# Kernel tuning notes

Measured on AMD Instinct MI355X. Metric: run time of the kernel, lower is better.

## Reference

```python
import jax, jax.numpy as jnp
import numpy as np

NUM_VIEWS = 11

def setup_inputs() -> dict:
    key = jax.random.key(0)
    ks = jax.random.split(key, 6)
    BF, T, D_IN, D_OUT, R = 128, 196, 1024, 1024, 4
    B = 16
    x = jax.random.normal(ks[0], (BF, T, D_IN), dtype=jnp.float32)
    view_idx = jax.random.randint(ks[1], (B,), 0, NUM_VIEWS)
    W = jax.random.normal(ks[2], (D_OUT, D_IN), dtype=jnp.float32) * (1.0 / np.sqrt(D_IN))
    b = jax.random.normal(ks[3], (D_OUT,), dtype=jnp.float32) * 0.01
    lora_A = jax.random.normal(ks[4], (NUM_VIEWS, D_IN, R), dtype=jnp.float32) * (1.0 / np.sqrt(D_IN))
    lora_B = jax.random.normal(ks[5], (NUM_VIEWS, R, D_OUT), dtype=jnp.float32) * 0.02
    return {"x": x, "view_idx": view_idx, "W": W, "b": b, "lora_A": lora_A, "lora_B": lora_B}

def reference(x, view_idx, W, b, lora_A, lora_B):
    # base linear: [BF, T, D_in] @ [D_in, D_out]
    out = jnp.einsum('bti,oi->bto', x, W) + b
    BF = x.shape[0]
    B = view_idx.shape[0]
    if BF != B:  # static shapes -> Python branch is jit-safe
        curr = jnp.repeat(view_idx, BF // B)  # expand per-frame view index
    else:
        curr = view_idx
    curr = jnp.clip(curr, 0, NUM_VIEWS - 1)
    A = lora_A[curr]          # [BF, D_in, R] gathered per sample
    Bm = lora_B[curr]         # [BF, R, D_out]
    h = jnp.einsum('bti,bir->btr', x, A)      # low-rank projection
    lora = jnp.einsum('btr,bro->bto', h, Bm)  # back to D_out
    return out + lora
```

## Files before the change

kernel.cpp:

```cpp
#include <hip/hip_runtime.h>
#include <hip/hip_bf16.h>
#include <stdint.h>

#define M_TOT 25088
#define N_TOT 1024
#define K_TOT 1024
#define NVIEW 11
#define ROWS_PER_VIEW 1568

#define BM 128
#define BN 128

typedef unsigned short u16;
typedef __bf16 bf16x8 __attribute__((ext_vector_type(8)));
typedef float f32x4 __attribute__((ext_vector_type(4)));
typedef unsigned short u16x4 __attribute__((ext_vector_type(4)));

#define AS1 __attribute__((address_space(1)))
#define AS3 __attribute__((address_space(3)))

#define XB_ELEMS ((size_t)M_TOT * K_TOT)
#define WB_ELEMS ((size_t)N_TOT * K_TOT)
#define WB_OFF_B (XB_ELEMS * 2)
#define H_OFF_B  (WB_OFF_B + WB_ELEMS * 2)
#define WS_NEEDED (H_OFF_B + (size_t)M_TOT * 4 * 4)

__device__ __forceinline__ u16 f2bf(float f) {
    union { float f; unsigned int i; } c; c.f = f;
    unsigned int i = c.i;
    return (u16)((i + 0x7FFFu + ((i >> 16) & 1u)) >> 16);
}

__global__ __launch_bounds__(256) void prep_kernel(
    const float* __restrict__ x, const float* __restrict__ W,
    const int* __restrict__ view_idx, const float* __restrict__ lora_A,
    u16* __restrict__ xb, u16* __restrict__ wb, float* __restrict__ h) {
    const int wave = threadIdx.x >> 6;
    const int lane = threadIdx.x & 63;
    const int blk  = blockIdx.x;

    if (blk >= M_TOT / 4) {
        const int row = (blk - M_TOT / 4) * 4 + wave;
        const float* src = W + (size_t)row * K_TOT;
        u16* dst = wb + (size_t)row * K_TOT;
#pragma unroll
        for (int it = 0; it < 4; ++it) {
            const int k = it * 256 + lane * 4;
            float4 v = *(const float4*)(src + k);
            u16x4 o = { f2bf(v.x), f2bf(v.y), f2bf(v.z), f2bf(v.w) };
            *(u16x4*)(dst + k) = o;
        }
        return;
    }

    const int row = blk * 4 + wave;
    int v = view_idx[row / ROWS_PER_VIEW];
    v = v < 0 ? 0 : (v > NVIEW - 1 ? NVIEW - 1 : v);
    const float* A  = lora_A + (size_t)v * (K_TOT * 4);
    const float* xr = x + (size_t)row * K_TOT;
    u16* dst = xb + (size_t)row * K_TOT;

    float a0 = 0.f, a1 = 0.f, a2 = 0.f, a3 = 0.f;
#pragma unroll
    for (int it = 0; it < 4; ++it) {
        const int k = it * 256 + lane * 4;
        float4 xv = *(const float4*)(xr + k);
        u16x4 o = { f2bf(xv.x), f2bf(xv.y), f2bf(xv.z), f2bf(xv.w) };
        *(u16x4*)(dst + k) = o;
        float4 av0 = *(const float4*)(A + (size_t)(k + 0) * 4);
        float4 av1 = *(const float4*)(A + (size_t)(k + 1) * 4);
        float4 av2 = *(const float4*)(A + (size_t)(k + 2) * 4);
        float4 av3 = *(const float4*)(A + (size_t)(k + 3) * 4);
        a0 += xv.x * av0.x + xv.y * av1.x + xv.z * av2.x + xv.w * av3.x;
        a1 += xv.x * av0.y + xv.y * av1.y + xv.z * av2.y + xv.w * av3.y;
        a2 += xv.x * av0.z + xv.y * av1.z + xv.z * av2.z + xv.w * av3.z;
        a3 += xv.x * av0.w + xv.y * av1.w + xv.z * av2.w + xv.w * av3.w;
    }
#pragma unroll
    for (int off = 32; off > 0; off >>= 1) {
        a0 += __shfl_xor(a0, off, 64);
        a1 += __shfl_xor(a1, off, 64);
        a2 += __shfl_xor(a2, off, 64);
        a3 += __shfl_xor(a3, off, 64);
    }
    if (lane == 0)
        *(float4*)(h + (size_t)row * 4) = make_float4(a0, a1, a2, a3);
}

__global__ __launch_bounds__(256) void h_only_kernel(
    const float* __restrict__ x, const int* __restrict__ view_idx,
    const float* __restrict__ lora_A, float* __restrict__ h) {
    const int row  = blockIdx.x * 4 + (threadIdx.x >> 6);
    const int lane = threadIdx.x & 63;
    int v = view_idx[row / ROWS_PER_VIEW];
    v = v < 0 ? 0 : (v > NVIEW - 1 ? NVIEW - 1 : v);
    const float* A  = lora_A + (size_t)v * (K_TOT * 4);
    const float* xr = x + (size_t)row * K_TOT;
    float a0 = 0.f, a1 = 0.f, a2 = 0.f, a3 = 0.f;
#pragma unroll
    for (int it = 0; it < 4; ++it) {
        const int k = it * 256 + lane * 4;
        float4 xv = *(const float4*)(xr + k);
        float4 av0 = *(const float4*)(A + (size_t)(k + 0) * 4);
        float4 av1 = *(const float4*)(A + (size_t)(k + 1) * 4);
        float4 av2 = *(const float4*)(A + (size_t)(k + 2) * 4);
        float4 av3 = *(const float4*)(A + (size_t)(k + 3) * 4);
        a0 += xv.x * av0.x + xv.y * av1.x + xv.z * av2.x + xv.w * av3.x;
        a1 += xv.x * av0.y + xv.y * av1.y + xv.z * av2.y + xv.w * av3.y;
        a2 += xv.x * av0.z + xv.y * av1.z + xv.z * av2.z + xv.w * av3.z;
        a3 += xv.x * av0.w + xv.y * av1.w + xv.z * av2.w + xv.w * av3.w;
    }
#pragma unroll
    for (int off = 32; off > 0; off >>= 1) {
        a0 += __shfl_xor(a0, off, 64);
        a1 += __shfl_xor(a1, off, 64);
        a2 += __shfl_xor(a2, off, 64);
        a3 += __shfl_xor(a3, off, 64);
    }
    if (lane == 0)
        *(float4*)(h + (size_t)row * 4) = make_float4(a0, a1, a2, a3);
}

__device__ __forceinline__ void stage32(const u16* __restrict__ gA,
                                        const u16* __restrict__ gB,
                                        u16* lA, u16* lB, int kofs, int tid) {
#pragma unroll
    for (int i = 0; i < 2; ++i) {
        const int e  = i * 2048 + tid * 8;
        const int r  = e >> 5;
        const int cc = tid & 3;
        const int c  = ((cc ^ ((r >> 1) & 3)) << 3);
        __builtin_amdgcn_global_load_lds(
            (const AS1 void*)(gA + (size_t)r * K_TOT + kofs + c),
            (AS3 void*)(lA + e), 16, 0, 0);
        __builtin_amdgcn_global_load_lds(
            (const AS1 void*)(gB + (size_t)r * K_TOT + kofs + c),
            (AS3 void*)(lB + e), 16, 0, 0);
    }
}

__global__ __launch_bounds__(256, 3) void gemm_bf16_kernel(
    const u16* __restrict__ xb, const u16* __restrict__ wb,
    const float* __restrict__ bias, const int* __restrict__ view_idx,
    const float* __restrict__ lora_B, const float* __restrict__ h,
    float* __restrict__ out) {
    __shared__ u16 As[2][BM * 32];
    __shared__ u16 Bs[2][BN * 32];

    const int tid = threadIdx.x;
    const int id = blockIdx.x;
    int bx, by;
    if (id < 1536) { const int c = id >> 6, w = id & 63; by = c * 8 + (w & 7); bx = w >> 3; }
    else           { const int r = id - 1536; by = 192 + (r & 3); bx = r >> 2; }

    const int lane = tid & 63;
    const int wave = tid >> 6;
    const int wm   = (wave >> 1) * 64;
    const int wn   = (wave & 1) * 64;
    const int l16  = lane & 15;
    const int quad = lane >> 4;
    const int sw2  = (l16 >> 1) & 3;
    const int csw  = ((quad ^ sw2) << 3);

    const u16* gA = xb + (size_t)(by * BM) * K_TOT;
    const u16* gB = wb + (size_t)(bx * BN) * K_TOT;

    f32x4 acc[4][4] = {};

    stage32(gA, gB, &As[0][0], &Bs[0][0], 0, tid);
    __syncthreads();

    #pragma unroll 2
    for (int kt = 0; kt < K_TOT / 32; ++kt) {
        const int buf  = kt & 1;
        const int nbuf = buf ^ 1;

        if (kt + 1 < K_TOT / 32)
            stage32(gA, gB, &As[nbuf][0], &Bs[nbuf][0], (kt + 1) * 32, tid);

        bf16x8 a_frag[4], b_frag[4];
#pragma unroll
        for (int mi = 0; mi < 4; ++mi)
            a_frag[mi] = *(const bf16x8*)(const void*)(
                &As[buf][0] + (wm + mi * 16 + l16) * 32 + csw);
#pragma unroll
        for (int ni = 0; ni < 4; ++ni)
            b_frag[ni] = *(const bf16x8*)(const void*)(
                &Bs[buf][0] + (wn + ni * 16 + l16) * 32 + csw);
#pragma unroll
        for (int mi = 0; mi < 4; ++mi)
#pragma unroll
            for (int ni = 0; ni < 4; ++ni)
                acc[mi][ni] = __builtin_amdgcn_mfma_f32_16x16x32_bf16(
                    a_frag[mi], b_frag[ni], acc[mi][ni], 0, 0, 0);

        __syncthreads();
    }

    const int rowBase = by * BM + wm;
    const int colBase = bx * BN + wn;
    float biasv[4];
#pragma unroll
    for (int ni = 0; ni < 4; ++ni) biasv[ni] = bias[colBase + ni * 16 + l16];

    const int ve0 = (by * BM) / ROWS_PER_VIEW;
    const int ve1 = (by * BM + BM - 1) / ROWS_PER_VIEW;
    if (ve0 == ve1) {
        int v = view_idx[ve0];
        v = v < 0 ? 0 : (v > NVIEW - 1 ? NVIEW - 1 : v);
        const float* Bv = lora_B + (size_t)v * (4 * N_TOT);
        float Bvv[4][4];
#pragma unroll
        for (int r = 0; r < 4; ++r)
#pragma unroll
            for (int ni = 0; ni < 4; ++ni)
                Bvv[r][ni] = Bv[r * N_TOT + colBase + ni * 16 + l16];
#pragma unroll
        for (int mi = 0; mi < 4; ++mi) {
#pragma unroll
            for (int reg = 0; reg < 4; ++reg) {
                const int grow = rowBase + mi * 16 + quad * 4 + reg;
                const float4 hv = *(const float4*)(h + (size_t)grow * 4);
                float* orow = out + (size_t)grow * N_TOT;
#pragma unroll
                for (int ni = 0; ni < 4; ++ni) {
                    float lora = hv.x * Bvv[0][ni] + hv.y * Bvv[1][ni]
                               + hv.z * Bvv[2][ni] + hv.w * Bvv[3][ni];
                    orow[colBase + ni * 16 + l16] = acc[mi][ni][reg] + biasv[ni] + lora;
                }
            }
        }
    } else {
#pragma unroll
        for (int mi = 0; mi < 4; ++mi) {
#pragma unroll
            for (int reg = 0; reg < 4; ++reg) {
                const int grow = rowBase + mi * 16 + quad * 4 + reg;
                int v = view_idx[grow / ROWS_PER_VIEW];
                v = v < 0 ? 0 : (v > NVIEW - 1 ? NVIEW - 1 : v);
                const float4 hv = *(const float4*)(h + (size_t)grow * 4);
                const float* Bv = lora_B + (size_t)v * (4 * N_TOT);
                float* orow = out + (size_t)grow * N_TOT;
#pragma unroll
                for (int ni = 0; ni < 4; ++ni) {
                    const int gcol = colBase + ni * 16 + l16;
                    float lora = hv.x * Bv[gcol]
                               + hv.y * Bv[N_TOT + gcol]
                               + hv.z * Bv[2 * N_TOT + gcol]
                               + hv.w * Bv[3 * N_TOT + gcol];
                    orow[gcol] = acc[mi][ni][reg] + biasv[ni] + lora;
                }
            }
        }
    }
}

__global__ __launch_bounds__(256, 3) void gemm_conv_kernel(
    const float* __restrict__ xp, const float* __restrict__ Wp,
    const float* __restrict__ bias, const int* __restrict__ view_idx,
    const float* __restrict__ lora_B, const float* __restrict__ h,
    float* __restrict__ out) {
    __shared__ u16 As[BM * 64];
    __shared__ u16 Bs[BN * 64];

    const int tid = threadIdx.x;
    const int id = blockIdx.x;
    int bx, by;
    if (id < 1536) { const int c = id >> 6, w = id & 63; by = c * 8 + (w & 7); bx = w >> 3; }
    else           { const int r = id - 1536; by = 192 + (r & 3); bx = r >> 2; }

    const int lane = tid & 63;
    const int wave = tid >> 6;
    const int wm   = (wave >> 1) * 64;
    const int wn   = (wave & 1) * 64;
    const int l16  = lane & 15;
    const int quad = lane >> 4;
    const int sw   = l16 & 7;

    const size_t a_base = (size_t)(by * BM) * K_TOT;
    const size_t b_base = (size_t)(bx * BN) * K_TOT;

    f32x4 acc[4][4] = {};

    for (int kt = 0; kt < K_TOT / 64; ++kt) {
        const int kofs = kt * 64;
#pragma unroll
        for (int i = 0; i < 8; ++i) {
            const int e = i * 1024 + tid * 4;
            const int r = e >> 6, o = e & 63;
            const int d = r * 64 + (((o >> 3) ^ (r & 7)) << 3) + (o & 7);
            float4 av = *(const float4*)(xp + a_base + (size_t)r * K_TOT + kofs + o);
            float4 bv = *(const float4*)(Wp + b_base + (size_t)r * K_TOT + kofs + o);
            u16x4 ao = { f2bf(av.x), f2bf(av.y), f2bf(av.z), f2bf(av.w) };
            u16x4 bo = { f2bf(bv.x), f2bf(bv.y), f2bf(bv.z), f2bf(bv.w) };
            *(u16x4*)(As + d) = ao;
            *(u16x4*)(Bs + d) = bo;
        }
        __syncthreads();
#pragma unroll
        for (int kk = 0; kk < 2; ++kk) {
            const int csw = (((kk * 4 + quad) ^ sw) << 3);
            bf16x8 a_frag[4], b_frag[4];
#pragma unroll
            for (int mi = 0; mi < 4; ++mi)
                a_frag[mi] = *(const bf16x8*)(const void*)(As + (wm + mi * 16 + l16) * 64 + csw);
#pragma unroll
            for (int ni = 0; ni < 4; ++ni)
                b_frag[ni] = *(const bf16x8*)(const void*)(Bs + (wn + ni * 16 + l16) * 64 + csw);
#pragma unroll
            for (int mi = 0; mi < 4; ++mi)
#pragma unroll
                for (int ni = 0; ni < 4; ++ni)
                    acc[mi][ni] = __builtin_amdgcn_mfma_f32_16x16x32_bf16(
                        a_frag[mi], b_frag[ni], acc[mi][ni], 0, 0, 0);
        }
        __syncthreads();
    }

    const int rowBase = by * BM + wm;
    const int colBase = bx * BN + wn;
    float biasv[4];
#pragma unroll
    for (int ni = 0; ni < 4; ++ni) biasv[ni] = bias[colBase + ni * 16 + l16];
#pragma unroll
    for (int mi = 0; mi < 4; ++mi) {
#pragma unroll
        for (int reg = 0; reg < 4; ++reg) {
            const int grow = rowBase + mi * 16 + quad * 4 + reg;
            int v = view_idx[grow / ROWS_PER_VIEW];
            v = v < 0 ? 0 : (v > NVIEW - 1 ? NVIEW - 1 : v);
            const float4 hv = *(const float4*)(h + (size_t)grow * 4);
            const float* Bv = lora_B + (size_t)v * (4 * N_TOT);
            float* orow = out + (size_t)grow * N_TOT;
#pragma unroll
            for (int ni = 0; ni < 4; ++ni) {
                const int gcol = colBase + ni * 16 + l16;
                float lora = hv.x * Bv[gcol]
                           + hv.y * Bv[N_TOT + gcol]
                           + hv.z * Bv[2 * N_TOT + gcol]
                           + hv.w * Bv[3 * N_TOT + gcol];
                orow[gcol] = acc[mi][ni][reg] + biasv[ni] + lora;
            }
        }
    }
}

extern "C" void kernel_launch(void* const* d_in, const int* in_sizes, int n_in,
                              void* d_out, int out_size, void* d_ws, size_t ws_size,
                              hipStream_t stream) {
    const float* x        = (const float*)d_in[0];
    const int*   view_idx = (const int*)d_in[1];
    const float* W        = (const float*)d_in[2];
    const float* b        = (const float*)d_in[3];
    const float* lora_A   = (const float*)d_in[4];
    const float* lora_B   = (const float*)d_in[5];
    float* out = (float*)d_out;

    const dim3 ggrid((M_TOT / BM) * (N_TOT / BN));
    if (ws_size >= WS_NEEDED) {
        u16*   xb = (u16*)d_ws;
        u16*   wb = (u16*)((char*)d_ws + WB_OFF_B);
        float* h  = (float*)((char*)d_ws + H_OFF_B);
        hipLaunchKernelGGL(prep_kernel, dim3(M_TOT / 4 + N_TOT / 4), dim3(256), 0, stream,
                           x, W, view_idx, lora_A, xb, wb, h);
        hipLaunchKernelGGL(gemm_bf16_kernel, ggrid, dim3(256), 0, stream,
                           xb, wb, b, view_idx, lora_B, h, out);
    } else {
        float* h = (float*)d_ws;
        hipLaunchKernelGGL(h_only_kernel, dim3(M_TOT / 4), dim3(256), 0, stream,
                           x, view_idx, lora_A, h);
        hipLaunchKernelGGL(gemm_conv_kernel, ggrid, dim3(256), 0, stream,
                           x, W, b, view_idx, lora_B, h, out);
    }
}
```

Measured before the change: 270.9 us.

## Enlarge bf16 GEMM tile to 256x128 with 512 threads and BK=64

The bf16 GEMM block grows to 256 rows by 128 columns with 8 waves, and K-staging moves to 64-wide single-buffered tiles with an XOR swizzle on 8 column groups. Block-to-tile mapping becomes an interleaved remap across 8 groups so consecutive blocks spread over the grid. The goal is more reuse of W tiles and fewer K-loop iterations and barriers. In exchange it drops the double buffering, so global loads no longer overlap with MFMA work within a block. The epilogue's per-view check now spans 256 rows, so more tiles may straddle view boundaries and take the slower path.

New measurement: 257.8 us. 1.05x faster.

```diff
diff --git a/kernel.cpp b/kernel.cpp
--- a/kernel.cpp
+++ b/kernel.cpp
@@ -8,8 +8,11 @@
 #define NVIEW 11
 #define ROWS_PER_VIEW 1568
 
-#define BM 128
+#define BM 256
 #define BN 128
+#define BK 64
+
+#define GRID_G ((M_TOT / BM) * (N_TOT / BN))
 
 typedef unsigned short u16;
 typedef __bf16 bf16x8 __attribute__((ext_vector_type(8)));
@@ -121,37 +124,42 @@
         *(float4*)(h + (size_t)row * 4) = make_float4(a0, a1, a2, a3);
 }
 
-__device__ __forceinline__ void stage32(const u16* __restrict__ gA,
-                                        const u16* __restrict__ gB,
-                                        u16* lA, u16* lB, int kofs, int tid) {
-#pragma unroll
-    for (int i = 0; i < 2; ++i) {
-        const int e  = i * 2048 + tid * 8;
-        const int r  = e >> 5;
-        const int cc = tid & 3;
-        const int c  = ((cc ^ ((r >> 1) & 3)) << 3);
+__device__ __forceinline__ void stage_tiles(const u16* __restrict__ gA,
+                                            const u16* __restrict__ gB,
+                                            u16* As, u16* Bs, int kofs, int tid) {
+#pragma unroll
+    for (int i = 0; i < 4; ++i) {
+        const int e = i * 4096 + tid * 8;
+        const int r = e >> 6;
+        const int c = (((tid & 7) ^ (r & 7)) << 3);
         __builtin_amdgcn_global_load_lds(
             (const AS1 void*)(gA + (size_t)r * K_TOT + kofs + c),
-            (AS3 void*)(lA + e), 16, 0, 0);
+            (AS3 void*)(As + e), 16, 0, 0);
+    }
+#pragma unroll
+    for (int i = 0; i < 2; ++i) {
+        const int e = i * 4096 + tid * 8;
+        const int r = e >> 6;
+        const int c = (((tid & 7) ^ (r & 7)) << 3);
         __builtin_amdgcn_global_load_lds(
             (const AS1 void*)(gB + (size_t)r * K_TOT + kofs + c),
-            (AS3 void*)(lB + e), 16, 0, 0);
-    }
-}
-
-__global__ __launch_bounds__(256, 3) void gemm_bf16_kernel(
+            (AS3 void*)(Bs + e), 16, 0, 0);
+    }
+}
+
+__global__ __launch_bounds__(512, 4) void gemm_bf16_kernel(
     const u16* __restrict__ xb, const u16* __restrict__ wb,
     const float* __restrict__ bias, const int* __restrict__ view_idx,
     const float* __restrict__ lora_B, const float* __restrict__ h,
     float* __restrict__ out) {
-    __shared__ u16 As[2][BM * 32];
-    __shared__ u16 Bs[2][BN * 32];
+    __shared__ u16 As[BM * BK];
+    __shared__ u16 Bs[BN * BK];
 
     const int tid = threadIdx.x;
-    const int id = blockIdx.x;
-    int bx, by;
-    if (id < 1536) { const int c = id >> 6, w = id & 63; by = c * 8 + (w & 7); bx = w >> 3; }
-    else           { const int r = id - 1536; by = 192 + (r & 3); bx = r >> 2; }
+    const int id   = blockIdx.x;
+    const int wgid = (id & 7) * (GRID_G / 8) + (id >> 3);
+    const int by   = wgid >> 3;
+    const int bx   = wgid & 7;
 
     const int lane = tid & 63;
     const int wave = tid >> 6;
@@ -159,41 +167,33 @@
     const int wn   = (wave & 1) * 64;
     const int l16  = lane & 15;
     const int quad = lane >> 4;
-    const int sw2  = (l16 >> 1) & 3;
-    const int csw  = ((quad ^ sw2) << 3);
+    const int sw   = l16 & 7;
 
     const u16* gA = xb + (size_t)(by * BM) * K_TOT;
     const u16* gB = wb + (size_t)(bx * BN) * K_TOT;
 
     f32x4 acc[4][4] = {};
 
-    stage32(gA, gB, &As[0][0], &Bs[0][0], 0, tid);
-    __syncthreads();
-
-    #pragma unroll 2
-    for (int kt = 0; kt < K_TOT / 32; ++kt) {
-        const int buf  = kt & 1;
-        const int nbuf = buf ^ 1;
-
-        if (kt + 1 < K_TOT / 32)
-            stage32(gA, gB, &As[nbuf][0], &Bs[nbuf][0], (kt + 1) * 32, tid);
-
-        bf16x8 a_frag[4], b_frag[4];
-#pragma unroll
-        for (int mi = 0; mi < 4; ++mi)
-            a_frag[mi] = *(const bf16x8*)(const void*)(
-                &As[buf][0] + (wm + mi * 16 + l16) * 32 + csw);
-#pragma unroll
-        for (int ni = 0; ni < 4; ++ni)
-            b_frag[ni] = *(const bf16x8*)(const void*)(
-                &Bs[buf][0] + (wn + ni * 16 + l16) * 32 + csw);
-#pragma unroll
-        for (int mi = 0; mi < 4; ++mi)
+    for (int kt = 0; kt < K_TOT / BK; ++kt) {
+        stage_tiles(gA, gB, As, Bs, kt * BK, tid);
+        __syncthreads();
+#pragma unroll
+        for (int kk = 0; kk < 2; ++kk) {
+            const int csw = (((kk * 4 + quad) ^ sw) << 3);
+            bf16x8 a_frag[4], b_frag[4];
+#pragma unroll
+            for (int mi = 0; mi < 4; ++mi)
+                a_frag[mi] = *(const bf16x8*)(const void*)(As + (wm + mi * 16 + l16) * BK + csw);
 #pragma unroll
             for (int ni = 0; ni < 4; ++ni)
-                acc[mi][ni] = __builtin_amdgcn_mfma_f32_16x16x32_bf16(
-                    a_frag[mi], b_frag[ni], acc[mi][ni], 0, 0, 0);
-
+                b_frag[ni] = *(const bf16x8*)(const void*)(Bs + (wn + ni * 16 + l16) * BK + csw);
+#pragma unroll
+            for (int mi = 0; mi < 4; ++mi)
+#pragma unroll
+                for (int ni = 0; ni < 4; ++ni)
+                    acc[mi][ni] = __builtin_amdgcn_mfma_f32_16x16x32_bf16(
+                        a_frag[mi], b_frag[ni], acc[mi][ni], 0, 0, 0);
+        }
         __syncthreads();
     }
 
@@ -260,8 +260,8 @@
     const float* __restrict__ bias, const int* __restrict__ view_idx,
     const float* __restrict__ lora_B, const float* __restrict__ h,
     float* __restrict__ out) {
-    __shared__ u16 As[BM * 64];
-    __shared__ u16 Bs[BN * 64];
+    __shared__ u16 As[128 * 64];
+    __shared__ u16 Bs[128 * 64];
 
     const int tid = threadIdx.x;
     const int id = blockIdx.x;
@@ -277,8 +277,8 @@
     const int quad = lane >> 4;
     const int sw   = l16 & 7;
 
-    const size_t a_base = (size_t)(by * BM) * K_TOT;
-    const size_t b_base = (size_t)(bx * BN) * K_TOT;
+    const size_t a_base = (size_t)(by * 128) * K_TOT;
+    const size_t b_base = (size_t)(bx * 128) * K_TOT;
 
     f32x4 acc[4][4] = {};
 
@@ -317,8 +317,8 @@
         __syncthreads();
     }
 
-    const int rowBase = by * BM + wm;
-    const int colBase = bx * BN + wn;
+    const int rowBase = by * 128 + wm;
+    const int colBase = bx * 128 + wn;
     float biasv[4];
 #pragma unroll
     for (int ni = 0; ni < 4; ++ni) biasv[ni] = bias[colBase + ni * 16 + l16];
@@ -356,20 +356,19 @@
     const float* lora_B   = (const float*)d_in[5];
     float* out = (float*)d_out;
 
-    const dim3 ggrid((M_TOT / BM) * (N_TOT / BN));
     if (ws_size >= WS_NEEDED) {
         u16*   xb = (u16*)d_ws;
         u16*   wb = (u16*)((char*)d_ws + WB_OFF_B);
         float* h  = (float*)((char*)d_ws + H_OFF_B);
         hipLaunchKernelGGL(prep_kernel, dim3(M_TOT / 4 + N_TOT / 4), dim3(256), 0, stream,
                            x, W, view_idx, lora_A, xb, wb, h);
-        hipLaunchKernelGGL(gemm_bf16_kernel, ggrid, dim3(256), 0, stream,
+        hipLaunchKernelGGL(gemm_bf16_kernel, dim3(GRID_G), dim3(512), 0, stream,
                            xb, wb, b, view_idx, lora_B, h, out);
     } else {
         float* h = (float*)d_ws;
         hipLaunchKernelGGL(h_only_kernel, dim3(M_TOT / 4), dim3(256), 0, stream,
                            x, view_idx, lora_A, h);
-        hipLaunchKernelGGL(gemm_conv_kernel, ggrid, dim3(256), 0, stream,
+        hipLaunchKernelGGL(gemm_conv_kernel, dim3((M_TOT / 128) * (N_TOT / 128)), dim3(256), 0, stream,
                            x, W, b, view_idx, lora_B, h, out);
     }
 }
```
